# Optimization experiments

Hardware: AMD Instinct MI355X
Metric: run time of the kernel (lower is better)

Reference implementation:

```python
import jax, jax.numpy as jnp
import numpy as np

NUM_HEADS = 16
HEAD_CH = 64
D_MODEL = 1024  # == NUM_HEADS*HEAD_CH -> out_mapper is Identity


def setup_inputs() -> dict:
    key = jax.random.key(0)
    k1, k2, k3 = jax.random.split(key, 3)
    tokens = jax.random.normal(k1, (2, 2048, D_MODEL), dtype=jnp.float32)
    w_qkv = jax.random.normal(k2, (D_MODEL, 3 * D_MODEL), dtype=jnp.float32) * (1.0 / np.sqrt(D_MODEL))
    b_qkv = jax.random.normal(k3, (3 * D_MODEL,), dtype=jnp.float32) * 0.02
    return {"tokens": tokens, "w_qkv": w_qkv, "b_qkv": b_qkv}


def reference(tokens, w_qkv, b_qkv):
    b, n, _ = tokens.shape
    qkv = tokens @ w_qkv + b_qkv  # [b, n, 3*inner]
    q, k, v = jnp.split(qkv, 3, axis=-1)

    def heads(x):  # [b, n, h*d] -> [b, h, n, d]
        return x.reshape(b, n, NUM_HEADS, HEAD_CH).transpose(0, 2, 1, 3)

    q, k, v = heads(q), heads(k), heads(v)
    scores = jnp.einsum('bhqd,bhkd->bhqk', q, k) / jnp.sqrt(jnp.float32(HEAD_CH))
    attn = jax.nn.softmax(scores, axis=-1)
    out = jnp.einsum('bhqk,bhkd->bhqd', attn, v)  # [b, h, n, d]
    out = out.transpose(0, 2, 1, 3).reshape(b, n, NUM_HEADS * HEAD_CH)
    return out  # out_mapper is Identity since inner_channels == input_channels
```

## Files before the change

kernel.cpp:

```cpp
#include <hip/hip_runtime.h>
#include <stdint.h>

typedef __attribute__((ext_vector_type(8))) short shortx8;
typedef __attribute__((ext_vector_type(4))) float floatx4;
typedef unsigned short bf16_t;

#define NH 16
#define HD 64
#define SEQ 2048
#define BATCH 2
#define DM 1024
#define DM3 3072

#define GLDS(gp, lp) __builtin_amdgcn_global_load_lds( \
    (const __attribute__((address_space(1))) unsigned int*)(gp), \
    (__attribute__((address_space(3))) unsigned int*)(lp), 16, 0, 0)

__device__ __forceinline__ bf16_t f2bf(float f) {
    unsigned int u = __float_as_uint(f);
    u += 0x7fff + ((u >> 16) & 1);
    return (bf16_t)(u >> 16);
}
__device__ __forceinline__ unsigned pk2bf(float lo, float hi) {
    return (unsigned)f2bf(lo) | ((unsigned)f2bf(hi) << 16);
}

__global__ __launch_bounds__(256) void conv_all(const float* __restrict__ tokens,
                                                bf16_t* __restrict__ tok_bf,
                                                const float* __restrict__ w,
                                                bf16_t* __restrict__ wt) {
    __shared__ bf16_t t[64 * 65];
    const int bx = blockIdx.x, tid = threadIdx.x;
    if (bx < 2048) {
        int idx = bx * 256 + tid;
        float4 a = ((const float4*)tokens)[idx * 2];
        float4 b = ((const float4*)tokens)[idx * 2 + 1];
        uint4 o;
        o.x = pk2bf(a.x, a.y);
        o.y = pk2bf(a.z, a.w);
        o.z = pk2bf(b.x, b.y);
        o.w = pk2bf(b.z, b.w);
        ((uint4*)tok_bf)[idx] = o;
    } else {
        const int bw = bx - 2048;
        const int n0 = (bw % 48) * 64, k0 = (bw / 48) * 64;
        for (int i = 0; i < 16; i++) {
            int idx = i * 256 + tid;
            int r = idx >> 6, c = idx & 63;
            t[r * 65 + c] = f2bf(w[(k0 + r) * DM3 + n0 + c]);
        }
        __syncthreads();
        for (int i = 0; i < 16; i++) {
            int idx = i * 256 + tid;
            int r = idx >> 6, c = idx & 63;
            wt[(n0 + r) * DM + k0 + c] = t[c * 65 + r];
        }
    }
}


#define QSCALE 0.18033688011f

template<bool SW>
__device__ __forceinline__ void kloop(const bf16_t* __restrict__ A, const bf16_t* __restrict__ Bt,
                                      bf16_t* __restrict__ As, bf16_t* __restrict__ Bs,
                                      int m0, int n0, floatx4 (&acc)[4][4]) {
    const int tid = threadIdx.x;
    const int wave = tid >> 6, lane = tid & 63;
    const int quad = lane >> 4, l16 = lane & 15;
    const int wm = (wave & 1) * 64, wn = (wave >> 1) * 64;
    const int srow = tid >> 3;
    const int swz8 = ((tid & 7) ^ (srow & 7)) * 8;
    const int h3 = l16 & 7;
    for (int kt = 0; kt < DM; kt += 64) {
        __syncthreads();
        for (int rr = 0; rr < 4; rr++) {
            GLDS(&A[(m0 + rr * 32 + srow) * DM + kt + swz8], &As[rr * 2048 + tid * 8]);
            GLDS(&Bt[(n0 + rr * 32 + srow) * DM + kt + swz8], &Bs[rr * 2048 + tid * 8]);
        }
        __syncthreads();
        for (int ks = 0; ks < 2; ks++) {
            const int g = ((ks * 4 + quad) ^ h3) * 8;
            shortx8 af[4], bfr[4];
            for (int t = 0; t < 4; t++)
                af[t] = *(const shortx8*)&As[(wm + t * 16 + l16) * 64 + g];
            for (int t = 0; t < 4; t++)
                bfr[t] = *(const shortx8*)&Bs[(wn + t * 16 + l16) * 64 + g];
            for (int i = 0; i < 4; i++)
                for (int j = 0; j < 4; j++)
                    acc[i][j] = SW
                        ? __builtin_amdgcn_mfma_f32_16x16x32_bf16(bfr[j], af[i], acc[i][j], 0, 0, 0)
                        : __builtin_amdgcn_mfma_f32_16x16x32_bf16(af[i], bfr[j], acc[i][j], 0, 0, 0);
        }
    }
}

__global__ __launch_bounds__(256) void qkv_gemm(const bf16_t* __restrict__ A,
                                                const bf16_t* __restrict__ Bt,
                                                const float* __restrict__ bias,
                                                bf16_t* __restrict__ Qo,
                                                bf16_t* __restrict__ Ko,
                                                bf16_t* __restrict__ Vto) {
    __shared__ __align__(16) char smem[128 * 136 * 2];
    bf16_t* As = (bf16_t*)smem;
    bf16_t* Bs = As + 128 * 64;
    bf16_t* Cs = (bf16_t*)smem;
    const int m0 = blockIdx.x * 128;
    const int n0 = blockIdx.y * 128;
    const int tid = threadIdx.x;
    const int wave = tid >> 6, lane = tid & 63;
    const int quad = lane >> 4, l16 = lane & 15;
    const int wm = (wave & 1) * 64, wn = (wave >> 1) * 64;
    const int part = n0 >> 10;
    const int b = m0 >> 11, pos0 = m0 & 2047;
    floatx4 acc[4][4] = {};

    if (part != 2) {
        kloop<true>(A, Bt, As, Bs, m0, n0, acc);
        __syncthreads();
        for (int i = 0; i < 4; i++) {
            int ml = wm + i * 16 + l16;
            for (int j = 0; j < 4; j++) {
                int nl = wn + j * 16 + quad * 4;
                float4 bv = *(const float4*)&bias[n0 + nl];
                float v0 = acc[i][j][0] + bv.x, v1 = acc[i][j][1] + bv.y;
                float v2 = acc[i][j][2] + bv.z, v3 = acc[i][j][3] + bv.w;
                if (part == 0) { v0 *= QSCALE; v1 *= QSCALE; v2 *= QSCALE; v3 *= QSCALE; }
                uint2 pk;
                pk.x = pk2bf(v0, v1);
                pk.y = pk2bf(v2, v3);
                *(uint2*)&Cs[ml * 136 + nl] = pk;
            }
        }
        __syncthreads();
        bf16_t* dst = (part == 0) ? Qo : Ko;
        for (int p = 0; p < 8; p++) {
            int ml = p * 16 + (tid >> 4);
            int g = tid & 15;
            uint4 v = *(const uint4*)&Cs[ml * 136 + g * 8];
            int rr = (n0 + g * 8) & 1023;
            int h = rr >> 6, d = rr & 63;
            *(uint4*)&dst[(size_t)((b * NH + h) * SEQ + pos0 + ml) * HD + d] = v;
        }
    } else {
        kloop<false>(A, Bt, As, Bs, m0, n0, acc);
        __syncthreads();
        for (int i = 0; i < 4; i++)
            for (int j = 0; j < 4; j++) {
                int nl = wn + j * 16 + l16;
                float bv = bias[n0 + nl];
                uint2 pk;
                pk.x = pk2bf(acc[i][j][0] + bv, acc[i][j][1] + bv);
                pk.y = pk2bf(acc[i][j][2] + bv, acc[i][j][3] + bv);
                *(uint2*)&Cs[nl * 136 + wm + i * 16 + quad * 4] = pk;
            }
        __syncthreads();
        for (int p = 0; p < 8; p++) {
            int nl = p * 16 + (tid >> 4);
            int g = tid & 15;
            uint4 v = *(const uint4*)&Cs[nl * 136 + g * 8];
            int rr = (n0 + nl) & 1023;
            int h = rr >> 6, d = rr & 63;
            *(uint4*)&Vto[(size_t)((b * NH + h) * HD + d) * SEQ + pos0 + g * 8] = v;
        }
    }
}

__global__ __launch_bounds__(256, 2) void attn(const bf16_t* __restrict__ Q,
                                               const bf16_t* __restrict__ K,
                                               const bf16_t* __restrict__ Vt,
                                               float* __restrict__ out) {
    __shared__ __align__(16) char smem[65536];
    bf16_t* Ks = (bf16_t*)smem;
    bf16_t* Vs = (bf16_t*)(smem + 16384);
    bf16_t* Ps = (bf16_t*)(smem + 32768);

    const int bh = blockIdx.x;
    const int qt_blk = blockIdx.y;
    const int b = bh >> 4, h = bh & 15;
    const int q0 = qt_blk * 128;
    const bf16_t* Qb = Q + ((size_t)bh * SEQ + q0) * HD;
    const bf16_t* Kb = K + (size_t)bh * SEQ * HD;
    const bf16_t* Vb = Vt + (size_t)bh * HD * SEQ;
    const int tid = threadIdx.x;
    const int wave = tid >> 6, lane = tid & 63;
    const int quad = lane >> 4, l16 = lane & 15;
    const int h3 = l16 & 7;
    const int qh = wave >> 1, kh = wave & 1;
    bf16_t* Pw = Ps + wave * 4096;

    const int srow = tid >> 3;
    const int sg8 = ((tid & 7) ^ (srow & 7)) * 8;
    const int vrow = tid >> 4;
    const int vg8 = (((tid & 15) ^ vrow) & 15) * 8;

    shortx8 qf[4][2];
    for (int qt = 0; qt < 4; qt++)
        for (int kc = 0; kc < 2; kc++)
            qf[qt][kc] = *(const shortx8*)&Qb[(qh * 64 + qt * 16 + l16) * 64 + kc * 32 + quad * 8];

    shortx8 ones;
    for (int i = 0; i < 8; i++) ones[i] = (short)0x3F80;

    const floatx4 minit = {-12.f, -12.f, -12.f, -12.f};
    floatx4 acc_l[4] = {};
    floatx4 acc_o[4][4] = {};

    for (int rr = 0; rr < 4; rr++) {
        GLDS(&Kb[(rr * 32 + srow) * 64 + sg8], &Ks[rr * 2048 + tid * 8]);
        GLDS(&Vb[(size_t)(rr * 16 + vrow) * SEQ + vg8], &Vs[rr * 2048 + tid * 8]);
    }
    __syncthreads();

    for (int it = 0; it < SEQ / 128; ++it) {
        shortx8 kf[2][4], vf[2][4];
        for (int kc = 0; kc < 2; kc++) {
            const int g = ((kc * 4 + quad) ^ h3) * 8;
            for (int kt = 0; kt < 4; kt++)
                kf[kc][kt] = *(const shortx8*)&Ks[(kh * 64 + kt * 16 + l16) * 64 + g];
        }
        for (int hp = 0; hp < 2; hp++)
            for (int dt = 0; dt < 4; dt++)
                vf[hp][dt] = *(const shortx8*)&Vs[(dt * 16 + l16) * 128 +
                                                  (((kh * 8 + hp * 4 + quad) ^ l16) & 15) * 8];
        __syncthreads();
        if (it + 1 < SEQ / 128) {
            const int kk = (it + 1) * 128;
            for (int rr = 0; rr < 4; rr++) {
                GLDS(&Kb[(kk + rr * 32 + srow) * 64 + sg8], &Ks[rr * 2048 + tid * 8]);
                GLDS(&Vb[(size_t)(rr * 16 + vrow) * SEQ + kk + vg8], &Vs[rr * 2048 + tid * 8]);
            }
        }

        for (int hp = 0; hp < 2; hp++) {
            floatx4 s[2][4];
            for (int k2 = 0; k2 < 2; k2++)
                for (int qt = 0; qt < 4; qt++) s[k2][qt] = minit;
            for (int kc = 0; kc < 2; kc++)
                for (int k2 = 0; k2 < 2; k2++)
                    for (int qt = 0; qt < 4; qt++)
                        s[k2][qt] = __builtin_amdgcn_mfma_f32_16x16x32_bf16(
                            kf[kc][hp * 2 + k2], qf[qt][kc], s[k2][qt], 0, 0, 0);
            for (int qt = 0; qt < 4; qt++)
                for (int k2 = 0; k2 < 2; k2++) {
                    unsigned u[4];
                    for (int r = 0; r < 4; r++)
                        u[r] = __float_as_uint(__builtin_amdgcn_exp2f(s[k2][qt][r])) + 0x8000u;
                    uint2 pk;
                    pk.x = __builtin_amdgcn_perm(u[1], u[0], 0x07060302u);
                    pk.y = __builtin_amdgcn_perm(u[3], u[2], 0x07060302u);
                    *(uint2*)&Pw[(qt * 16 + l16) * 64 +
                                 (((hp * 2 + k2) * 2 + (quad >> 1)) ^ h3) * 8 + (quad & 1) * 4] = pk;
                }
            const int gp = ((hp * 4 + quad) ^ h3) * 8;
            for (int qt = 0; qt < 4; qt++) {
                shortx8 pf = *(const shortx8*)&Pw[(qt * 16 + l16) * 64 + gp];
                acc_l[qt] = __builtin_amdgcn_mfma_f32_16x16x32_bf16(ones, pf, acc_l[qt], 0, 0, 0);
                for (int dt = 0; dt < 4; dt++)
                    acc_o[dt][qt] = __builtin_amdgcn_mfma_f32_16x16x32_bf16(vf[hp][dt], pf, acc_o[dt][qt], 0, 0, 0);
            }
        }
        __syncthreads();
    }

    float* Osh = (float*)smem;
    float* ml = (float*)(smem + 32768);
    if (kh == 1) {
        for (int qt = 0; qt < 4; qt++) {
            for (int dt = 0; dt < 4; dt++) {
                float4 o;
                o.x = acc_o[dt][qt][0]; o.y = acc_o[dt][qt][1];
                o.z = acc_o[dt][qt][2]; o.w = acc_o[dt][qt][3];
                *(float4*)&Osh[qh * 4096 + (qt * 16 + l16) * 64 +
                               (((dt * 4 + quad) ^ l16) & 15) * 4] = o;
            }
            if (quad == 0) ml[(qh * 4 + qt) * 16 + l16] = acc_l[qt][0];
        }
    }
    __syncthreads();
    if (kh == 0) {
        for (int qt = 0; qt < 4; qt++) {
            float l1 = ml[(qh * 4 + qt) * 16 + l16];
            float inv = 1.0f / (acc_l[qt][0] + l1);
            int q = q0 + qh * 64 + qt * 16 + l16;
            for (int dt = 0; dt < 4; dt++) {
                float4 o1 = *(const float4*)&Osh[qh * 4096 + (qt * 16 + l16) * 64 +
                                                 (((dt * 4 + quad) ^ l16) & 15) * 4];
                float4 o;
                o.x = (acc_o[dt][qt][0] + o1.x) * inv;
                o.y = (acc_o[dt][qt][1] + o1.y) * inv;
                o.z = (acc_o[dt][qt][2] + o1.z) * inv;
                o.w = (acc_o[dt][qt][3] + o1.w) * inv;
                *(float4*)&out[(size_t)(b * SEQ + q) * DM + h * HD + dt * 16 + quad * 4] = o;
            }
        }
    }
}

extern "C" void kernel_launch(void* const* d_in, const int* in_sizes, int n_in,
                              void* d_out, int out_size, void* d_ws, size_t ws_size,
                              hipStream_t stream) {
    const float* tokens = (const float*)d_in[0];
    const float* w = (const float*)d_in[1];
    const float* bias = (const float*)d_in[2];
    float* out = (float*)d_out;
    char* ws = (char*)d_ws;

    bf16_t* tok_bf = (bf16_t*)(ws);
    bf16_t* wt_bf  = (bf16_t*)(ws + (size_t)8 * 1024 * 1024);
    bf16_t* Qb     = (bf16_t*)(ws + (size_t)14 * 1024 * 1024);
    bf16_t* Kb     = (bf16_t*)(ws + (size_t)22 * 1024 * 1024);
    bf16_t* Vb     = (bf16_t*)(ws + (size_t)30 * 1024 * 1024);

    conv_all<<<2816, 256, 0, stream>>>(tokens, tok_bf, w, wt_bf);
    qkv_gemm<<<dim3(32, 24), 256, 0, stream>>>(tok_bf, wt_bf, bias, Qb, Kb, Vb);
    attn<<<dim3(32, 16), 256, 0, stream>>>(Qb, Kb, Vb, out);
}
```

Baseline: 163.2 us.

## Rewrite QKV GEMM with 256x256 tiles and double-buffered LDS pipeline

The QKV projection GEMM moves from 128x128 tiles with 4 waves to 256x256 tiles with 8 waves. Its K loop becomes a double-buffered pipeline built on direct global-to-LDS loads, explicit vmcnt/lgkmcnt waits, raw barriers and s_setprio around the MFMA bursts, so tile loads overlap with matrix math. The epilogue staging buffer switches from padded rows to an XOR-swizzled layout. The grid shrinks to 192 blocks, which may leave CUs idle, and 128KB of LDS per block limits residency to one block per CU.

```diff
diff --git a/kernel.cpp b/kernel.cpp
--- a/kernel.cpp
+++ b/kernel.cpp
@@ -15,6 +15,11 @@
 #define GLDS(gp, lp) __builtin_amdgcn_global_load_lds( \
     (const __attribute__((address_space(1))) unsigned int*)(gp), \
     (__attribute__((address_space(3))) unsigned int*)(lp), 16, 0, 0)
+
+#define BARX() __builtin_amdgcn_s_barrier()
+#define VMCNT(n) asm volatile("s_waitcnt vmcnt(" #n ")" ::: "memory")
+#define LGKM0() do { asm volatile("s_waitcnt lgkmcnt(0)" ::: "memory"); \
+                     __builtin_amdgcn_sched_barrier(0); } while (0)
 
 __device__ __forceinline__ bf16_t f2bf(float f) {
     unsigned int u = __float_as_uint(f);
@@ -61,106 +66,193 @@
 
 #define QSCALE 0.18033688011f
 
+__device__ __forceinline__ void stage_half(const bf16_t* __restrict__ g0,
+                                           bf16_t* lds) {
+    GLDS(g0, lds);
+    GLDS(g0 + (size_t)64 * DM, lds + 4096);
+}
+
+template<int MH>
+__device__ __forceinline__ void rd_a(const bf16_t* As, int slot, int arow,
+                                     int kg0, int kg1, shortx8 (&af)[4][2]) {
+#pragma unroll
+    for (int t = 0; t < 4; t++) {
+        const bf16_t* p = &As[slot * 16384 + arow + (MH * 4 + t) * 2048];
+        af[t][0] = *(const shortx8*)(p + kg0);
+        af[t][1] = *(const shortx8*)(p + kg1);
+    }
+}
+
+template<int NHH>
+__device__ __forceinline__ void rd_b(const bf16_t* Bs, int slot, int brow,
+                                     int kg0, int kg1, shortx8 (&bfr)[4][2]) {
+#pragma unroll
+    for (int t = 0; t < 2; t++) {
+        const bf16_t* p = &Bs[slot * 16384 + brow + (NHH * 2 + t) * 4096];
+        bfr[NHH * 2 + t][0] = *(const shortx8*)(p + kg0);
+        bfr[NHH * 2 + t][1] = *(const shortx8*)(p + kg1);
+    }
+}
+
+template<bool SW, int MH, int NHH>
+__device__ __forceinline__ void mfmaq(const shortx8 (&af)[4][2], const shortx8 (&bfr)[4][2],
+                                      floatx4 (&acc)[8][4]) {
+    __builtin_amdgcn_s_setprio(1);
+#pragma unroll
+    for (int i = 0; i < 4; i++)
+#pragma unroll
+        for (int j = 0; j < 2; j++) {
+#pragma unroll
+            for (int ks = 0; ks < 2; ks++)
+                acc[MH * 4 + i][NHH * 2 + j] = SW
+                    ? __builtin_amdgcn_mfma_f32_16x16x32_bf16(bfr[NHH * 2 + j][ks], af[i][ks],
+                                                              acc[MH * 4 + i][NHH * 2 + j], 0, 0, 0)
+                    : __builtin_amdgcn_mfma_f32_16x16x32_bf16(af[i][ks], bfr[NHH * 2 + j][ks],
+                                                              acc[MH * 4 + i][NHH * 2 + j], 0, 0, 0);
+        }
+    __builtin_amdgcn_s_setprio(0);
+}
+
 template<bool SW>
-__device__ __forceinline__ void kloop(const bf16_t* __restrict__ A, const bf16_t* __restrict__ Bt,
-                                      bf16_t* __restrict__ As, bf16_t* __restrict__ Bs,
-                                      int m0, int n0, floatx4 (&acc)[4][4]) {
+__device__ __forceinline__ void kloop256(const bf16_t* __restrict__ A,
+                                         const bf16_t* __restrict__ Bt,
+                                         char* smem, int m0, int n0,
+                                         floatx4 (&acc)[8][4]) {
     const int tid = threadIdx.x;
-    const int wave = tid >> 6, lane = tid & 63;
+    const int lane = tid & 63, wave = tid >> 6;
+    const int wr = wave >> 2, wc = wave & 3;
     const int quad = lane >> 4, l16 = lane & 15;
-    const int wm = (wave & 1) * 64, wn = (wave >> 1) * 64;
+    const int h3 = l16 & 7;
+    bf16_t* As = (bf16_t*)smem;
+    bf16_t* Bs = (bf16_t*)(smem + 65536);
     const int srow = tid >> 3;
-    const int swz8 = ((tid & 7) ^ (srow & 7)) * 8;
-    const int h3 = l16 & 7;
-    for (int kt = 0; kt < DM; kt += 64) {
-        __syncthreads();
-        for (int rr = 0; rr < 4; rr++) {
-            GLDS(&A[(m0 + rr * 32 + srow) * DM + kt + swz8], &As[rr * 2048 + tid * 8]);
-            GLDS(&Bt[(n0 + rr * 32 + srow) * DM + kt + swz8], &Bs[rr * 2048 + tid * 8]);
-        }
-        __syncthreads();
-        for (int ks = 0; ks < 2; ks++) {
-            const int g = ((ks * 4 + quad) ^ h3) * 8;
-            shortx8 af[4], bfr[4];
-            for (int t = 0; t < 4; t++)
-                af[t] = *(const shortx8*)&As[(wm + t * 16 + l16) * 64 + g];
-            for (int t = 0; t < 4; t++)
-                bfr[t] = *(const shortx8*)&Bs[(wn + t * 16 + l16) * 64 + g];
-            for (int i = 0; i < 4; i++)
-                for (int j = 0; j < 4; j++)
-                    acc[i][j] = SW
-                        ? __builtin_amdgcn_mfma_f32_16x16x32_bf16(bfr[j], af[i], acc[i][j], 0, 0, 0)
-                        : __builtin_amdgcn_mfma_f32_16x16x32_bf16(af[i], bfr[j], acc[i][j], 0, 0, 0);
-        }
-    }
-}
-
-__global__ __launch_bounds__(256) void qkv_gemm(const bf16_t* __restrict__ A,
-                                                const bf16_t* __restrict__ Bt,
-                                                const float* __restrict__ bias,
-                                                bf16_t* __restrict__ Qo,
-                                                bf16_t* __restrict__ Ko,
-                                                bf16_t* __restrict__ Vto) {
-    __shared__ __align__(16) char smem[128 * 136 * 2];
-    bf16_t* As = (bf16_t*)smem;
-    bf16_t* Bs = As + 128 * 64;
-    bf16_t* Cs = (bf16_t*)smem;
-    const int m0 = blockIdx.x * 128;
-    const int n0 = blockIdx.y * 128;
+    const int sg8 = ((tid & 7) ^ (srow & 7)) * 8;
+    const bf16_t* Ag = A + (size_t)(m0 + srow) * DM + sg8;
+    const bf16_t* Bg = Bt + (size_t)(n0 + srow) * DM + sg8;
+
+    const int kg0 = (quad ^ h3) * 8;
+    const int kg1 = ((4 + quad) ^ h3) * 8;
+    const int arow = (wr * 16 + l16) * 64;
+    const int brow = (wc * 16 + l16) * 64;
+
+    shortx8 af[4][2], bfr[4][2];
+
+    stage_half(Ag,                            &As[tid * 8]);
+    stage_half(Bg,                            &Bs[tid * 8]);
+    stage_half(Ag + (size_t)128 * DM,         &As[8192 + tid * 8]);
+    stage_half(Bg + (size_t)128 * DM,         &Bs[8192 + tid * 8]);
+    stage_half(Ag + 64,                       &As[16384 + tid * 8]);
+    stage_half(Bg + 64,                       &Bs[16384 + tid * 8]);
+    VMCNT(8);
+    BARX();
+
+    for (int t = 0; t < 16; ++t) {
+        const int s = t & 1;
+        const int t1 = (t + 1) & 15, t2 = (t + 2) & 15;
+        rd_a<0>(As, s, arow, kg0, kg1, af);
+        rd_b<0>(Bs, s, brow, kg0, kg1, bfr);
+        stage_half(Ag + (size_t)128 * DM + t1 * 64, &As[(s ^ 1) * 16384 + 8192 + tid * 8]);
+        VMCNT(6);
+        BARX(); LGKM0();
+        mfmaq<SW, 0, 0>(af, bfr, acc);
+        BARX();
+        rd_b<1>(Bs, s, brow, kg0, kg1, bfr);
+        stage_half(Bg + (size_t)128 * DM + t1 * 64, &Bs[(s ^ 1) * 16384 + 8192 + tid * 8]);
+        BARX(); LGKM0();
+        mfmaq<SW, 0, 1>(af, bfr, acc);
+        BARX();
+        rd_a<1>(As, s, arow, kg0, kg1, af);
+        stage_half(Ag + t2 * 64, &As[s * 16384 + tid * 8]);
+        BARX(); LGKM0();
+        mfmaq<SW, 1, 0>(af, bfr, acc);
+        BARX();
+        stage_half(Bg + t2 * 64, &Bs[s * 16384 + tid * 8]);
+        VMCNT(8);
+        BARX();
+        mfmaq<SW, 1, 1>(af, bfr, acc);
+        BARX();
+    }
+}
+
+__global__ __launch_bounds__(512, 2) void qkv_gemm(const bf16_t* __restrict__ A,
+                                                   const bf16_t* __restrict__ Bt,
+                                                   const float* __restrict__ bias,
+                                                   bf16_t* __restrict__ Qo,
+                                                   bf16_t* __restrict__ Ko,
+                                                   bf16_t* __restrict__ Vto) {
+    __shared__ __align__(16) char smem[131072];
+    const int m0 = blockIdx.x * 256;
+    const int n0 = blockIdx.y * 256;
     const int tid = threadIdx.x;
-    const int wave = tid >> 6, lane = tid & 63;
+    const int lane = tid & 63, wave = tid >> 6;
+    const int wr = wave >> 2, wc = wave & 3;
     const int quad = lane >> 4, l16 = lane & 15;
-    const int wm = (wave & 1) * 64, wn = (wave >> 1) * 64;
     const int part = n0 >> 10;
     const int b = m0 >> 11, pos0 = m0 & 2047;
-    floatx4 acc[4][4] = {};
+    floatx4 acc[8][4] = {};
 
     if (part != 2) {
-        kloop<true>(A, Bt, As, Bs, m0, n0, acc);
-        __syncthreads();
-        for (int i = 0; i < 4; i++) {
-            int ml = wm + i * 16 + l16;
-            for (int j = 0; j < 4; j++) {
-                int nl = wn + j * 16 + quad * 4;
-                float4 bv = *(const float4*)&bias[n0 + nl];
-                float v0 = acc[i][j][0] + bv.x, v1 = acc[i][j][1] + bv.y;
-                float v2 = acc[i][j][2] + bv.z, v3 = acc[i][j][3] + bv.w;
+        kloop256<true>(A, Bt, smem, m0, n0, acc);
+        asm volatile("s_waitcnt vmcnt(0)" ::: "memory");
+        __syncthreads();
+        bf16_t* Cs = (bf16_t*)smem;
+#pragma unroll
+        for (int mf = 0; mf < 8; mf++) {
+            int m = wr * 16 + mf * 32 + l16;
+            char* rowp = (char*)Cs + m * 512;
+            int sw = (m & 7) << 4;
+#pragma unroll
+            for (int nf = 0; nf < 4; nf++) {
+                int n = wc * 16 + nf * 64 + quad * 4;
+                float4 bv = *(const float4*)&bias[n0 + n];
+                float v0 = acc[mf][nf][0] + bv.x, v1 = acc[mf][nf][1] + bv.y;
+                float v2 = acc[mf][nf][2] + bv.z, v3 = acc[mf][nf][3] + bv.w;
                 if (part == 0) { v0 *= QSCALE; v1 *= QSCALE; v2 *= QSCALE; v3 *= QSCALE; }
                 uint2 pk;
                 pk.x = pk2bf(v0, v1);
                 pk.y = pk2bf(v2, v3);
-                *(uint2*)&Cs[ml * 136 + nl] = pk;
+                *(uint2*)(rowp + ((n * 2) ^ sw)) = pk;
             }
         }
         __syncthreads();
         bf16_t* dst = (part == 0) ? Qo : Ko;
-        for (int p = 0; p < 8; p++) {
-            int ml = p * 16 + (tid >> 4);
-            int g = tid & 15;
-            uint4 v = *(const uint4*)&Cs[ml * 136 + g * 8];
-            int rr = (n0 + g * 8) & 1023;
-            int h = rr >> 6, d = rr & 63;
-            *(uint4*)&dst[(size_t)((b * NH + h) * SEQ + pos0 + ml) * HD + d] = v;
+#pragma unroll
+        for (int it = 0; it < 16; it++) {
+            int c = it * 512 + tid;
+            int m = c >> 5, g = c & 31;
+            uint4 v = *(const uint4*)((char*)Cs + m * 512 + ((g * 16) ^ ((m & 7) << 4)));
+            int ng = n0 + g * 8;
+            int h = (ng >> 6) & 15, d = ng & 63;
+            *(uint4*)&dst[(size_t)((b * NH + h) * SEQ + pos0 + m) * HD + d] = v;
         }
     } else {
-        kloop<false>(A, Bt, As, Bs, m0, n0, acc);
-        __syncthreads();
-        for (int i = 0; i < 4; i++)
-            for (int j = 0; j < 4; j++) {
-                int nl = wn + j * 16 + l16;
-                float bv = bias[n0 + nl];
+        kloop256<false>(A, Bt, smem, m0, n0, acc);
+        asm volatile("s_waitcnt vmcnt(0)" ::: "memory");
+        __syncthreads();
+        bf16_t* Cs = (bf16_t*)smem;
+#pragma unroll
+        for (int nf = 0; nf < 4; nf++) {
+            int n = wc * 16 + nf * 64 + l16;
+            float bv = bias[n0 + n];
+            char* rowp = (char*)Cs + n * 512;
+            int sw = (n & 7) << 4;
+#pragma unroll
+            for (int mf = 0; mf < 8; mf++) {
+                int m = wr * 16 + mf * 32 + quad * 4;
                 uint2 pk;
-                pk.x = pk2bf(acc[i][j][0] + bv, acc[i][j][1] + bv);
-                pk.y = pk2bf(acc[i][j][2] + bv, acc[i][j][3] + bv);
-                *(uint2*)&Cs[nl * 136 + wm + i * 16 + quad * 4] = pk;
-            }
-        __syncthreads();
-        for (int p = 0; p < 8; p++) {
-            int nl = p * 16 + (tid >> 4);
-            int g = tid & 15;
-            uint4 v = *(const uint4*)&Cs[nl * 136 + g * 8];
-            int rr = (n0 + nl) & 1023;
-            int h = rr >> 6, d = rr & 63;
+                pk.x = pk2bf(acc[mf][nf][0] + bv, acc[mf][nf][1] + bv);
+                pk.y = pk2bf(acc[mf][nf][2] + bv, acc[mf][nf][3] + bv);
+                *(uint2*)(rowp + ((m * 2) ^ sw)) = pk;
+            }
+        }
+        __syncthreads();
+#pragma unroll
+        for (int it = 0; it < 16; it++) {
+            int c = it * 512 + tid;
+            int n = c >> 5, g = c & 31;
+            uint4 v = *(const uint4*)((char*)Cs + n * 512 + ((g * 16) ^ ((n & 7) << 4)));
+            int ng = n0 + n;
+            int h = (ng >> 6) & 15, d = ng & 63;
             *(uint4*)&Vto[(size_t)((b * NH + h) * HD + d) * SEQ + pos0 + g * 8] = v;
         }
     }
@@ -313,6 +405,6 @@
     bf16_t* Vb     = (bf16_t*)(ws + (size_t)30 * 1024 * 1024);
 
     conv_all<<<2816, 256, 0, stream>>>(tokens, tok_bf, w, wt_bf);
-    qkv_gemm<<<dim3(32, 24), 256, 0, stream>>>(tok_bf, wt_bf, bias, Qb, Kb, Vb);
+    qkv_gemm<<<dim3(16, 12), 512, 0, stream>>>(tok_bf, wt_bf, bias, Qb, Kb, Vb);
     attn<<<dim3(32, 16), 256, 0, stream>>>(Qb, Kb, Vb, out);
 }
```

Result: faster. 155.6 us (-4.7%).
